# Kernel optimization log

Measured on AMD Instinct MI355X. Metric: run time of the kernel, lower is better.

The kernel has to match this reference:

```python
import jax, jax.numpy as jnp
import numpy as np
from jax import lax

K = 5        # kernel size
STRIDE = 1
DN = ('NCHW', 'OIHW', 'NCHW')


def _dist_conv(x, w):
    """Euclidean distance between every kxk window of x [B,1,H,W] and each
    filter w [O,1,k,k] -> [B,O,Hout,Wout].  Uses the identity
    ||p - w||^2 = sum(p^2) - 2 p.w + ||w||^2 so the cross term is one conv."""
    xw = lax.conv_general_dilated(x, w, (STRIDE, STRIDE), 'VALID',
                                  dimension_numbers=DN)
    ones = jnp.ones((1, 1, K, K), x.dtype)
    x2 = lax.conv_general_dilated(x * x, ones, (STRIDE, STRIDE), 'VALID',
                                  dimension_numbers=DN)
    w2 = jnp.sum(w * w, axis=(1, 2, 3))[None, :, None, None]
    d2 = jnp.maximum(x2 - 2.0 * xw + w2, 1e-12)  # clamp for sqrt stability
    return jnp.sqrt(d2)


def setup_inputs() -> dict:
    key = jax.random.key(0)
    k1, k2, k3, k4 = jax.random.split(key, 4)
    B, H, W, O = 16, 112, 112, 256
    gray_input = jax.random.normal(k1, (B, 1, H, W), jnp.float32)
    rgb_input = jax.random.normal(k2, (B, 1, H, W), jnp.float32)
    # kaiming-uniform-like init, first filter zeroed (as in reset_parameters)
    bound = 1.0 / np.sqrt(K * K)
    gray_weight = jax.random.uniform(k3, (O, 1, K, K), jnp.float32, -bound, bound)
    gray_weight = gray_weight.at[0].set(0.0)
    rgb_weight = jax.random.uniform(k4, (O, 1, K, K), jnp.float32, -bound, bound)
    rgb_weight = rgb_weight.at[0].set(0.0)
    std = jnp.asarray(2.0, jnp.float32)
    return {"gray_input": gray_input, "rgb_input": rgb_input,
            "gray_weight": gray_weight, "rgb_weight": rgb_weight, "std": std}


def reference(gray_input, rgb_input, gray_weight, rgb_weight, std):
    d = _dist_conv(gray_input, gray_weight) + _dist_conv(rgb_input, rgb_weight)
    # gaussian RBF on the summed distances
    return jnp.exp(-(d * d) / (2.0 * std * std))
```

## Files before the change

kernel.cpp:

```cpp
#include <hip/hip_runtime.h>
#include <math.h>

#define BB    16
#define HH    112
#define IMSZ  (HH*HH)
#define OO    256
#define OHW   108
#define PLANE (OHW*OHW)
#define MTOTAL (BB*PLANE)
#define MTILE 256
#define WRECB 144
#define WRECW 36
#define NXCD  8

typedef __attribute__((ext_vector_type(8))) short short8;
typedef __attribute__((ext_vector_type(4))) float f32x4;

__device__ __forceinline__ unsigned short f2bf(float x) {
    unsigned u = __builtin_bit_cast(unsigned, x);
    return (unsigned short)((u + 0x7fffu + ((u >> 16) & 1u)) >> 16);
}
__device__ __forceinline__ float bf2f(unsigned short h) {
    unsigned u = ((unsigned)h) << 16;
    return __builtin_bit_cast(float, u);
}

__global__ __launch_bounds__(512)
void dist_rbf_mfma(const float* __restrict__ gx, const float* __restrict__ rx,
                   const float* __restrict__ gw, const float* __restrict__ rw,
                   const float* __restrict__ stdp, float* __restrict__ out)
{
    __shared__ __align__(16) unsigned wrec[2 * OO * WRECW];
    __shared__ float w2s[2 * OO];

    const int tid = threadIdx.x;

    const int nwg = gridDim.x;
    const int hw  = blockIdx.x;
    const int xcd = hw % NXCD, idx = hw / NXCD;
    const int q = nwg / NXCD, r = nwg % NXCD;
    const int lb = (xcd < r ? xcd * (q + 1) : r * (q + 1) + (xcd - r) * q) + idx;

    {
        const int img = tid >> 8;
        const int o   = tid & 255;
        const float* wsrc = img ? rw : gw;
        unsigned* rec = wrec + img * OO * WRECW + o * WRECW;
        float v[32]; unsigned short h[32];
        float s = 0.f;
        #pragma unroll
        for (int i = 0; i < 32; i++) {
            float x = (i < 25) ? wsrc[o * 25 + i] : 0.f;
            v[i] = x; s = fmaf(x, x, s); h[i] = f2bf(x);
        }
        w2s[img * OO + o] = s;
        #pragma unroll
        for (int wd = 0; wd < 16; wd++) {
            rec[wd] = (unsigned)h[2*wd] | ((unsigned)h[2*wd+1] << 16);
            unsigned short l0 = f2bf(v[2*wd]   - bf2f(h[2*wd]));
            unsigned short l1 = f2bf(v[2*wd+1] - bf2f(h[2*wd+1]));
            rec[16 + wd] = (unsigned)l0 | ((unsigned)l1 << 16);
        }
    }
    __syncthreads();

    const int lid  = tid & 63;
    const int wid  = tid >> 6;
    const int mcol = lid & 15;
    const int kgrp = lid >> 4;
    const int k0   = kgrp * 8;

    const float sd   = stdp[0];
    const float kneg = -1.f / (2.f * sd * sd);

    const int pbase = lb * MTILE;

    short8 ah[2][2], al[2][2];
    float  x2v[2][2][4];

    #pragma unroll
    for (int mf = 0; mf < 2; mf++) {
        const int p  = pbase + (wid * 2 + mf) * 16 + mcol;
        const int b  = p / PLANE;
        const int pp = p - b * PLANE;
        const int oh = pp / OHW;
        const int ow = pp - oh * OHW;
        const size_t ibase = (size_t)b * IMSZ + oh * HH + ow;
        #pragma unroll
        for (int img = 0; img < 2; img++) {
            const float* src = (img == 0 ? gx : rx) + ibase;
            float xs[8];
            float part = 0.f;
            #pragma unroll
            for (int j = 0; j < 8; j++) {
                int k = k0 + j;
                int r2 = k / 5, c2 = k - r2 * 5;
                float x = (k < 25) ? src[r2 * HH + c2] : 0.f;
                xs[j] = x; part = fmaf(x, x, part);
            }
            part += __shfl_xor(part, 16);
            part += __shfl_xor(part, 32);
            #pragma unroll
            for (int rr = 0; rr < 4; rr++)
                x2v[mf][img][rr] = __shfl(part, kgrp * 4 + rr);
            short8 hi, lo;
            #pragma unroll
            for (int j = 0; j < 8; j++) {
                unsigned short hh = f2bf(xs[j]);
                hi[j] = (short)hh;
                lo[j] = (short)f2bf(xs[j] - bf2f(hh));
            }
            ah[mf][img] = hi; al[mf][img] = lo;
        }
    }

    const char* wrecB = (const char*)wrec;
    #pragma unroll 2
    for (int ot = 0; ot < 16; ot++) {
        const int o = ot * 16 + mcol;
        const char* recg = wrecB + (size_t)o * WRECB + kgrp * 16;
        const char* recr = recg + (size_t)OO * WRECB;
        short8 bhg = *(const short8*)recg;
        short8 blg = *(const short8*)(recg + 64);
        short8 bhr = *(const short8*)recr;
        short8 blr = *(const short8*)(recr + 64);
        const float w2g = w2s[o];
        const float w2r = w2s[OO + o];

        #pragma unroll
        for (int mf = 0; mf < 2; mf++) {
            f32x4 cg = {0.f, 0.f, 0.f, 0.f};
            f32x4 cr = {0.f, 0.f, 0.f, 0.f};
            cg = __builtin_amdgcn_mfma_f32_16x16x32_bf16(ah[mf][0], bhg, cg, 0, 0, 0);
            cg = __builtin_amdgcn_mfma_f32_16x16x32_bf16(ah[mf][0], blg, cg, 0, 0, 0);
            cg = __builtin_amdgcn_mfma_f32_16x16x32_bf16(al[mf][0], bhg, cg, 0, 0, 0);
            cr = __builtin_amdgcn_mfma_f32_16x16x32_bf16(ah[mf][1], bhr, cr, 0, 0, 0);
            cr = __builtin_amdgcn_mfma_f32_16x16x32_bf16(ah[mf][1], blr, cr, 0, 0, 0);
            cr = __builtin_amdgcn_mfma_f32_16x16x32_bf16(al[mf][1], bhr, cr, 0, 0, 0);

            f32x4 res;
            #pragma unroll
            for (int rr = 0; rr < 4; rr++) {
                float d2g = fmaf(-2.f, cg[rr], x2v[mf][0][rr] + w2g);
                float d2r = fmaf(-2.f, cr[rr], x2v[mf][1][rr] + w2r);
                d2g = fmaxf(d2g, 1e-12f);
                d2r = fmaxf(d2r, 1e-12f);
                float d2 = fmaf(2.f, __builtin_amdgcn_sqrtf(d2g * d2r), d2g + d2r);
                res[rr] = __expf(kneg * d2);
            }
            const int prow0 = pbase + (wid * 2 + mf) * 16 + kgrp * 4;
            const int b0  = prow0 / PLANE;
            const int pp0 = prow0 - b0 * PLANE;
            *(f32x4*)(out + ((size_t)(b0 * OO + o)) * PLANE + pp0) = res;
        }
    }
}

extern "C" void kernel_launch(void* const* d_in, const int* in_sizes, int n_in,
                              void* d_out, int out_size, void* d_ws, size_t ws_size,
                              hipStream_t stream) {
    const float* gx   = (const float*)d_in[0];
    const float* rx   = (const float*)d_in[1];
    const float* gw   = (const float*)d_in[2];
    const float* rw   = (const float*)d_in[3];
    const float* stdp = (const float*)d_in[4];
    float* out = (float*)d_out;

    dim3 grid(MTOTAL / MTILE, 1, 1);
    dim3 block(512, 1, 1);
    dist_rbf_mfma<<<grid, block, 0, stream>>>(gx, rx, gw, rw, stdp, out);
}
```

Before: 50.29 us.

## Use 1024-thread blocks looping over three sub-tiles to amortize weight staging

Each workgroup now has 16 waves of one 16-row M fragment each, and loops over three consecutive 256-pixel sub-tiles. The grid shrinks by a factor of three. The goal is to amortize the per-block LDS weight preparation (bf16 hi/lo split and squared norms) across more output pixels. In exchange it gives up the two-fragment reuse of each weight LDS load within a wave, and the larger blocks may lower occupancy or cause tail imbalance.

```diff
diff --git a/kernel.cpp b/kernel.cpp
--- a/kernel.cpp
+++ b/kernel.cpp
@@ -9,6 +9,7 @@
 #define PLANE (OHW*OHW)
 #define MTOTAL (BB*PLANE)
 #define MTILE 256
+#define KSUB  3
 #define WRECB 144
 #define WRECW 36
 #define NXCD  8
@@ -25,7 +26,7 @@
     return __builtin_bit_cast(float, u);
 }
 
-__global__ __launch_bounds__(512)
+__global__ __launch_bounds__(1024)
 void dist_rbf_mfma(const float* __restrict__ gx, const float* __restrict__ rx,
                    const float* __restrict__ gw, const float* __restrict__ rw,
                    const float* __restrict__ stdp, float* __restrict__ out)
@@ -41,7 +42,7 @@
     const int q = nwg / NXCD, r = nwg % NXCD;
     const int lb = (xcd < r ? xcd * (q + 1) : r * (q + 1) + (xcd - r) * q) + idx;
 
-    {
+    if (tid < 2 * OO) {
         const int img = tid >> 8;
         const int o   = tid & 255;
         const float* wsrc = img ? rw : gw;
@@ -72,83 +73,81 @@
 
     const float sd   = stdp[0];
     const float kneg = -1.f / (2.f * sd * sd);
+    const char* wrecB = (const char*)wrec;
 
-    const int pbase = lb * MTILE;
+    for (int st = 0; st < KSUB; st++) {
+        const int pbase = (lb * KSUB + st) * MTILE;
 
-    short8 ah[2][2], al[2][2];
-    float  x2v[2][2][4];
+        short8 ah[2], al[2];
+        float  x2v[2][4];
 
-    #pragma unroll
-    for (int mf = 0; mf < 2; mf++) {
-        const int p  = pbase + (wid * 2 + mf) * 16 + mcol;
-        const int b  = p / PLANE;
-        const int pp = p - b * PLANE;
-        const int oh = pp / OHW;
-        const int ow = pp - oh * OHW;
-        const size_t ibase = (size_t)b * IMSZ + oh * HH + ow;
-        #pragma unroll
-        for (int img = 0; img < 2; img++) {
-            const float* src = (img == 0 ? gx : rx) + ibase;
-            float xs[8];
-            float part = 0.f;
+        {
+            const int p  = pbase + wid * 16 + mcol;
+            const int b  = p / PLANE;
+            const int pp = p - b * PLANE;
+            const int oh = pp / OHW;
+            const int ow = pp - oh * OHW;
+            const size_t ibase = (size_t)b * IMSZ + oh * HH + ow;
             #pragma unroll
-            for (int j = 0; j < 8; j++) {
-                int k = k0 + j;
-                int r2 = k / 5, c2 = k - r2 * 5;
-                float x = (k < 25) ? src[r2 * HH + c2] : 0.f;
-                xs[j] = x; part = fmaf(x, x, part);
+            for (int img = 0; img < 2; img++) {
+                const float* src = (img == 0 ? gx : rx) + ibase;
+                float xs[8];
+                float part = 0.f;
+                #pragma unroll
+                for (int j = 0; j < 8; j++) {
+                    int k = k0 + j;
+                    int r2 = k / 5, c2 = k - r2 * 5;
+                    float x = (k < 25) ? src[r2 * HH + c2] : 0.f;
+                    xs[j] = x; part = fmaf(x, x, part);
+                }
+                part += __shfl_xor(part, 16);
+                part += __shfl_xor(part, 32);
+                #pragma unroll
+                for (int rr = 0; rr < 4; rr++)
+                    x2v[img][rr] = __shfl(part, kgrp * 4 + rr);
+                short8 hi, lo;
+                #pragma unroll
+                for (int j = 0; j < 8; j++) {
+                    unsigned short hh = f2bf(xs[j]);
+                    hi[j] = (short)hh;
+                    lo[j] = (short)f2bf(xs[j] - bf2f(hh));
+                }
+                ah[img] = hi; al[img] = lo;
             }
-            part += __shfl_xor(part, 16);
-            part += __shfl_xor(part, 32);
-            #pragma unroll
-            for (int rr = 0; rr < 4; rr++)
-                x2v[mf][img][rr] = __shfl(part, kgrp * 4 + rr);
-            short8 hi, lo;
-            #pragma unroll
-            for (int j = 0; j < 8; j++) {
-                unsigned short hh = f2bf(xs[j]);
-                hi[j] = (short)hh;
-                lo[j] = (short)f2bf(xs[j] - bf2f(hh));
-            }
-            ah[mf][img] = hi; al[mf][img] = lo;
         }
-    }
 
-    const char* wrecB = (const char*)wrec;
-    #pragma unroll 2
-    for (int ot = 0; ot < 16; ot++) {
-        const int o = ot * 16 + mcol;
-        const char* recg = wrecB + (size_t)o * WRECB + kgrp * 16;
-        const char* recr = recg + (size_t)OO * WRECB;
-        short8 bhg = *(const short8*)recg;
-        short8 blg = *(const short8*)(recg + 64);
-        short8 bhr = *(const short8*)recr;
-        short8 blr = *(const short8*)(recr + 64);
-        const float w2g = w2s[o];
-        const float w2r = w2s[OO + o];
+        #pragma unroll 2
+        for (int ot = 0; ot < 16; ot++) {
+            const int o = ot * 16 + mcol;
+            const char* recg = wrecB + (size_t)o * WRECB + kgrp * 16;
+            const char* recr = recg + (size_t)OO * WRECB;
+            short8 bhg = *(const short8*)recg;
+            short8 blg = *(const short8*)(recg + 64);
+            short8 bhr = *(const short8*)recr;
+            short8 blr = *(const short8*)(recr + 64);
+            const float w2g = w2s[o];
+            const float w2r = w2s[OO + o];
 
-        #pragma unroll
-        for (int mf = 0; mf < 2; mf++) {
             f32x4 cg = {0.f, 0.f, 0.f, 0.f};
             f32x4 cr = {0.f, 0.f, 0.f, 0.f};
-            cg = __builtin_amdgcn_mfma_f32_16x16x32_bf16(ah[mf][0], bhg, cg, 0, 0, 0);
-            cg = __builtin_amdgcn_mfma_f32_16x16x32_bf16(ah[mf][0], blg, cg, 0, 0, 0);
-            cg = __builtin_amdgcn_mfma_f32_16x16x32_bf16(al[mf][0], bhg, cg, 0, 0, 0);
-            cr = __builtin_amdgcn_mfma_f32_16x16x32_bf16(ah[mf][1], bhr, cr, 0, 0, 0);
-            cr = __builtin_amdgcn_mfma_f32_16x16x32_bf16(ah[mf][1], blr, cr, 0, 0, 0);
-            cr = __builtin_amdgcn_mfma_f32_16x16x32_bf16(al[mf][1], bhr, cr, 0, 0, 0);
+            cg = __builtin_amdgcn_mfma_f32_16x16x32_bf16(ah[0], bhg, cg, 0, 0, 0);
+            cg = __builtin_amdgcn_mfma_f32_16x16x32_bf16(ah[0], blg, cg, 0, 0, 0);
+            cg = __builtin_amdgcn_mfma_f32_16x16x32_bf16(al[0], bhg, cg, 0, 0, 0);
+            cr = __builtin_amdgcn_mfma_f32_16x16x32_bf16(ah[1], bhr, cr, 0, 0, 0);
+            cr = __builtin_amdgcn_mfma_f32_16x16x32_bf16(ah[1], blr, cr, 0, 0, 0);
+            cr = __builtin_amdgcn_mfma_f32_16x16x32_bf16(al[1], bhr, cr, 0, 0, 0);
 
             f32x4 res;
             #pragma unroll
             for (int rr = 0; rr < 4; rr++) {
-                float d2g = fmaf(-2.f, cg[rr], x2v[mf][0][rr] + w2g);
-                float d2r = fmaf(-2.f, cr[rr], x2v[mf][1][rr] + w2r);
+                float d2g = fmaf(-2.f, cg[rr], x2v[0][rr] + w2g);
+                float d2r = fmaf(-2.f, cr[rr], x2v[1][rr] + w2r);
                 d2g = fmaxf(d2g, 1e-12f);
                 d2r = fmaxf(d2r, 1e-12f);
                 float d2 = fmaf(2.f, __builtin_amdgcn_sqrtf(d2g * d2r), d2g + d2r);
                 res[rr] = __expf(kneg * d2);
             }
-            const int prow0 = pbase + (wid * 2 + mf) * 16 + kgrp * 4;
+            const int prow0 = pbase + wid * 16 + kgrp * 4;
             const int b0  = prow0 / PLANE;
             const int pp0 = prow0 - b0 * PLANE;
             *(f32x4*)(out + ((size_t)(b0 * OO + o)) * PLANE + pp0) = res;
@@ -166,7 +165,7 @@
     const float* stdp = (const float*)d_in[4];
     float* out = (float*)d_out;
 
-    dim3 grid(MTOTAL / MTILE, 1, 1);
-    dim3 block(512, 1, 1);
+    dim3 grid(MTOTAL / (MTILE * KSUB), 1, 1);
+    dim3 block(1024, 1, 1);
     dist_rbf_mfma<<<grid, block, 0, stream>>>(gx, rx, gw, rw, stdp, out);
 }
```

New measurement: 46.66 us. -7.2%, faster.
